# Kernel optimization log

Measured on AMD Instinct MI355X. Metric: run time of the kernel, lower is better.

## Reference

```python
import jax, jax.numpy as jnp
import numpy as np

N, E = 50000, 800000          # nodes, directed edges
F_IN = 80                     # 16 unique sensors * 5 features
H, C = 4, 96                  # num_heads, hidden_dim
D = H * C                     # 384 = concat output dim per GAT layer
NC = 20                       # n_classes = number of components
NEG_SLOPE = 0.2               # PyG GATv2Conv default negative_slope
EPS = 1e-5                    # LayerNorm eps


def layer_norm(x, g, b):
    mu = x.mean(-1, keepdims=True)
    var = x.var(-1, keepdims=True)
    return (x - mu) * jax.lax.rsqrt(var + EPS) * g + b


def gatv2(x, src, dst, Wsrc, Wdst, att, bias):
    # GATv2Conv (concat=True): e_ij = att . leaky_relu(Wsrc x_j + Wdst x_i),
    # alpha = segment-softmax over dst, out_i = sum_j alpha_ij * (Wsrc x_j)
    n = x.shape[0]
    xs = (x @ Wsrc).reshape(n, H, C)
    xd = (x @ Wdst).reshape(n, H, C)
    m = jax.nn.leaky_relu(xs[src] + xd[dst], NEG_SLOPE)      # [E,H,C]
    e = jnp.einsum('ehc,hc->eh', m, att)                     # [E,H]
    emax = jax.ops.segment_max(e, dst, num_segments=n)       # [N,H]
    ex = jnp.exp(e - emax[dst])
    denom = jax.ops.segment_sum(ex, dst, num_segments=n)
    alpha = ex / (denom[dst] + 1e-16)                        # [E,H]
    out = jax.ops.segment_sum(alpha[:, :, None] * xs[src], dst, num_segments=n)
    return out.reshape(n, D) + bias


def setup_inputs():
    key = jax.random.key(0)
    ks = jax.random.split(key, 16)

    def w(k, shape, fan):
        return (jax.random.normal(k, shape, jnp.float32) / np.float32(np.sqrt(fan)))

    inp = {
        'x': jax.random.normal(ks[0], (N, F_IN), jnp.float32),
        'edge_index': jax.random.randint(ks[1], (2, E), 0, N, jnp.int32),
    }
    dims = [F_IN, D, D]
    i = 2
    for l in range(3):
        inp[f'Wsrc{l}'] = w(ks[i], (dims[l], D), dims[l]); i += 1
        inp[f'Wdst{l}'] = w(ks[i], (dims[l], D), dims[l]); i += 1
        inp[f'att{l}'] = w(ks[i], (H, C), C); i += 1
        inp[f'b{l}'] = jnp.zeros((D,), jnp.float32)
        inp[f'g{l}'] = jnp.ones((D,), jnp.float32)
        inp[f'be{l}'] = jnp.zeros((D,), jnp.float32)
    inp['Wc1'] = w(ks[i], (D, C), D); i += 1
    inp['bc1'] = jnp.zeros((C,), jnp.float32)
    inp['gc'] = jnp.ones((C,), jnp.float32)
    inp['bec'] = jnp.zeros((C,), jnp.float32)
    inp['Wc2'] = w(ks[i], (C, NC), C)
    inp['bc2'] = jnp.zeros((NC,), jnp.float32)
    return inp


def reference(x, edge_index,
              Wsrc0, Wdst0, att0, b0, g0, be0,
              Wsrc1, Wdst1, att1, b1, g1, be1,
              Wsrc2, Wdst2, att2, b2, g2, be2,
              Wc1, bc1, gc, bec, Wc2, bc2):
    src, dst = edge_index[0], edge_index[1]
    layers = [(Wsrc0, Wdst0, att0, b0, g0, be0),
              (Wsrc1, Wdst1, att1, b1, g1, be1),
              (Wsrc2, Wdst2, att2, b2, g2, be2)]
    h = x
    for (Ws, Wd, a, b, g, be) in layers:
        h = gatv2(h, src, dst, Ws, Wd, a, b)
        h = jax.nn.elu(layer_norm(h, g, be))   # dropout: identity in eval mode
    h = jax.nn.relu(h @ Wc1 + bc1)
    h = layer_norm(h, gc, bec)
    return h @ Wc2 + bc2
```

## Files before the change

kernel.cpp:

```cpp
#include <hip/hip_runtime.h>
#include <math.h>

#define D 384
#define NCLS 20
#define FIN 80
#define CH 96

typedef unsigned int u32t;
typedef unsigned short u16t;
typedef __attribute__((ext_vector_type(8))) short bf16x8;
typedef __attribute__((ext_vector_type(4))) float f32x4;

__device__ __forceinline__ u16t f2bf(float f) {
    u32t b = __float_as_uint(f);
    u32t r = (b + 0x7FFFu + ((b >> 16) & 1u)) >> 16;
    return (u16t)r;
}
__device__ __forceinline__ float bfl(u32t u) { return __uint_as_float(u << 16); }
__device__ __forceinline__ float bfh(u32t u) { return __uint_as_float(u & 0xFFFF0000u); }

#define GLOAD16(g, l)                                                            \
    __builtin_amdgcn_global_load_lds(                                            \
        (const __attribute__((address_space(1))) void*)(g),                      \
        (__attribute__((address_space(3))) void*)(l), 16, 0, 0)


__global__ void k_zero(int* p, int n) {
    int i = blockIdx.x * blockDim.x + threadIdx.x;
    if (i < n) p[i] = 0;
}

__global__ void k_hist(const int* __restrict__ dst, int* __restrict__ deg, int E) {
    int i = blockIdx.x * blockDim.x + threadIdx.x;
    if (i < E) atomicAdd(&deg[dst[i]], 1);
}

__global__ __launch_bounds__(256) void k_scan1(const int* __restrict__ deg,
                                               int* __restrict__ offs,
                                               int* __restrict__ bsum, int n) {
    __shared__ int sh[256];
    int t = threadIdx.x, i = blockIdx.x * 256 + t;
    int v = (i < n) ? deg[i] : 0;
    sh[t] = v;
    __syncthreads();
    for (int o = 1; o < 256; o <<= 1) {
        int a = (t >= o) ? sh[t - o] : 0;
        __syncthreads();
        sh[t] += a;
        __syncthreads();
    }
    if (i < n) offs[i] = sh[t] - v;
    if (t == 255) bsum[blockIdx.x] = sh[255];
}

__global__ __launch_bounds__(256) void k_scan2(int* __restrict__ bsum, int nb,
                                               int* __restrict__ offs, int n) {
    __shared__ int sh[256];
    int t = threadIdx.x;
    int v = (t < nb) ? bsum[t] : 0;
    sh[t] = v;
    __syncthreads();
    for (int o = 1; o < 256; o <<= 1) {
        int a = (t >= o) ? sh[t - o] : 0;
        __syncthreads();
        sh[t] += a;
        __syncthreads();
    }
    if (t < nb) bsum[t] = sh[t] - v;
    if (t == 255) offs[n] = sh[255];
}

__global__ __launch_bounds__(256) void k_scan3(int* __restrict__ offs,
                                               int* __restrict__ cursor,
                                               const int* __restrict__ bsum, int n) {
    int i = blockIdx.x * 256 + threadIdx.x;
    if (i < n) {
        int o = offs[i] + bsum[blockIdx.x];
        offs[i] = o;
        cursor[i] = o;
    }
}

__global__ void k_scatter(const int* __restrict__ src, const int* __restrict__ dst,
                          int* __restrict__ cursor, int* __restrict__ csr_srcb, int E) {
    int i = blockIdx.x * blockDim.x + threadIdx.x;
    if (i < E) {
        int p = atomicAdd(&cursor[dst[i]], 1);
        csr_srcb[p] = src[i] * 384;
    }
}


__global__ void k_cvt_x(const float* __restrict__ x, u16t* __restrict__ xbf, int N) {
    int i = blockIdx.x * 256 + threadIdx.x;
    if (i >= N * 96) return;
    int r = i / 96, c = i - r * 96;
    float v = (c < FIN) ? x[r * FIN + c] : 0.f;
    xbf[i] = f2bf(v);
}

__global__ void k_cvt_wT(const float* __restrict__ W, u16t* __restrict__ WT,
                         int K, int Kp) {
    int i = blockIdx.x * 256 + threadIdx.x;
    if (i >= D * Kp) return;
    int c = i / Kp, k = i - c * Kp;
    float v = (k < K) ? W[(size_t)k * D + c] : 0.f;
    WT[i] = f2bf(v);
}

__global__ void k_cvt_wc1T(const float* __restrict__ W, u16t* __restrict__ WT) {
    int i = blockIdx.x * 256 + threadIdx.x;
    if (i >= 128 * D) return;
    int c = i / D, k = i - c * D;
    float v = (c < CH) ? W[(size_t)k * CH + c] : 0.f;
    WT[i] = f2bf(v);
}


__global__ __launch_bounds__(256) void k_mm(const u16t* __restrict__ A,
                                            const u16t* __restrict__ BT,
                                            u16t* __restrict__ C, int Kp, int ostride) {
    __shared__ u16t Al[4][128][8];
    __shared__ u16t Bl[4][128][8];
    const int t = threadIdx.x;
    const int wave = t >> 6, lane = t & 63;
    const int wr = wave >> 1, wc = wave & 1;
    const int bm0 = blockIdx.x * 128;
    const int bn0 = blockIdx.y * 128;
    const int col16 = lane & 15, kc = lane >> 4;

    f32x4 acc[4][4] = {};

    const u16t* asrc0 = A + (size_t)(bm0 + lane) * Kp + wave * 8;
    const u16t* asrc1 = A + (size_t)(bm0 + 64 + lane) * Kp + wave * 8;
    const u16t* bsrc0 = BT + (size_t)(bn0 + lane) * Kp + wave * 8;
    const u16t* bsrc1 = BT + (size_t)(bn0 + 64 + lane) * Kp + wave * 8;
    u16t* alds0 = &Al[wave][0][0];
    u16t* alds1 = &Al[wave][64][0];
    u16t* blds0 = &Bl[wave][0][0];
    u16t* blds1 = &Bl[wave][64][0];

    for (int k0 = 0; k0 < Kp; k0 += 32) {
        GLOAD16(asrc0 + k0, alds0);
        GLOAD16(asrc1 + k0, alds1);
        GLOAD16(bsrc0 + k0, blds0);
        GLOAD16(bsrc1 + k0, blds1);
        __syncthreads();

        bf16x8 a[4], b[4];
#pragma unroll
        for (int m = 0; m < 4; m++)
            a[m] = *(const bf16x8*)&Al[kc][wr * 64 + m * 16 + col16][0];
#pragma unroll
        for (int n = 0; n < 4; n++)
            b[n] = *(const bf16x8*)&Bl[kc][wc * 64 + n * 16 + col16][0];
#pragma unroll
        for (int m = 0; m < 4; m++)
#pragma unroll
            for (int n = 0; n < 4; n++)
                acc[m][n] = __builtin_amdgcn_mfma_f32_16x16x32_bf16(
                    a[m], b[n], acc[m][n], 0, 0, 0);
        __syncthreads();
    }

#pragma unroll
    for (int m = 0; m < 4; m++) {
#pragma unroll
        for (int n = 0; n < 4; n++) {
#pragma unroll
            for (int j = 0; j < 4; j++) {
                int row = bm0 + wr * 64 + m * 16 + (lane >> 4) * 4 + j;
                int col = bn0 + wc * 64 + n * 16 + col16;
                C[(size_t)row * ostride + col] = f2bf(acc[m][n][j]);
            }
        }
    }
}


__global__ __launch_bounds__(256) void k_mmh(const u16t* __restrict__ A,
                                             const u16t* __restrict__ BT,
                                             const float* __restrict__ bc1,
                                             float* __restrict__ Yh) {
    __shared__ u16t Al[4][128][8];
    __shared__ u16t Bl[4][128][8];
    const int t = threadIdx.x;
    const int wave = t >> 6, lane = t & 63;
    const int wr = wave >> 1, wc = wave & 1;
    const int bm0 = blockIdx.x * 128;
    const int col16 = lane & 15, kc = lane >> 4;

    f32x4 acc[4][4] = {};

    const u16t* asrc0 = A + (size_t)(bm0 + lane) * D + wave * 8;
    const u16t* asrc1 = A + (size_t)(bm0 + 64 + lane) * D + wave * 8;
    const u16t* bsrc0 = BT + (size_t)lane * D + wave * 8;
    const u16t* bsrc1 = BT + (size_t)(64 + lane) * D + wave * 8;
    u16t* alds0 = &Al[wave][0][0];
    u16t* alds1 = &Al[wave][64][0];
    u16t* blds0 = &Bl[wave][0][0];
    u16t* blds1 = &Bl[wave][64][0];

    for (int k0 = 0; k0 < D; k0 += 32) {
        GLOAD16(asrc0 + k0, alds0);
        GLOAD16(asrc1 + k0, alds1);
        GLOAD16(bsrc0 + k0, blds0);
        GLOAD16(bsrc1 + k0, blds1);
        __syncthreads();

        bf16x8 a[4], b[4];
#pragma unroll
        for (int m = 0; m < 4; m++)
            a[m] = *(const bf16x8*)&Al[kc][wr * 64 + m * 16 + col16][0];
#pragma unroll
        for (int n = 0; n < 4; n++)
            b[n] = *(const bf16x8*)&Bl[kc][wc * 64 + n * 16 + col16][0];
#pragma unroll
        for (int m = 0; m < 4; m++)
#pragma unroll
            for (int n = 0; n < 4; n++)
                acc[m][n] = __builtin_amdgcn_mfma_f32_16x16x32_bf16(
                    a[m], b[n], acc[m][n], 0, 0, 0);
        __syncthreads();
    }

#pragma unroll
    for (int m = 0; m < 4; m++) {
#pragma unroll
        for (int n = 0; n < 4; n++) {
            int col = wc * 64 + n * 16 + col16;
            if (col < CH) {
                float bc = bc1[col];
#pragma unroll
                for (int j = 0; j < 4; j++) {
                    int row = bm0 + wr * 64 + m * 16 + (lane >> 4) * 4 + j;
                    Yh[(size_t)row * CH + col] = fmaxf(acc[m][n][j] + bc, 0.f);
                }
            }
        }
    }
}


__global__ __launch_bounds__(256) void k_gat(const u32t* __restrict__ XSXD,
                                             const float* __restrict__ att,
                                             const float* __restrict__ bias,
                                             const float* __restrict__ gamma,
                                             const float* __restrict__ beta,
                                             const int* __restrict__ offs,
                                             const int* __restrict__ csr_srcb,
                                             u16t* __restrict__ Hout,
                                             int N) {
    int wave = threadIdx.x >> 6;
    int lane = threadIdx.x & 63;
    int node = blockIdx.x * 4 + wave;
    if (node >= N) return;
    int c0 = lane * 6;
    int lo3 = lane * 3;

    const u32t* xdp = XSXD + (size_t)node * 384 + 192 + lo3;
    u32t d0 = xdp[0], d1 = xdp[1], d2 = xdp[2];
    float xd[6] = {bfl(d0), bfh(d0), bfl(d1), bfh(d1), bfl(d2), bfh(d2)};
    float attr[6];
#pragma unroll
    for (int k = 0; k < 6; k++) attr[k] = att[c0 + k];

    float m = -INFINITY, denom = 0.f;
    float acc[6] = {0.f, 0.f, 0.f, 0.f, 0.f, 0.f};
    int e0 = offs[node], e1 = offs[node + 1];

    for (int e = e0; e < e1; e++) {
        const u32t* xsp = XSXD + (u32t)csr_srcb[e] + lo3;
        u32t a0 = xsp[0], a1 = xsp[1], a2 = xsp[2];
        float xs[6] = {bfl(a0), bfh(a0), bfl(a1), bfh(a1), bfl(a2), bfh(a2)};
        float part = 0.f;
#pragma unroll
        for (int k = 0; k < 6; k++) {
            float v = xs[k] + xd[k];
            part = fmaf(fmaxf(v, 0.2f * v), attr[k], part);
        }
#pragma unroll
        for (int o = 1; o < 16; o <<= 1) part += __shfl_xor(part, o, 64);

        if (__builtin_expect(__any(part - m > 8.0f), 0)) {
            float nm = fmaxf(m, part);
            float r = __expf(m - nm);
            float p = __expf(part - nm);
            denom = denom * r + p;
#pragma unroll
            for (int k = 0; k < 6; k++) acc[k] = fmaf(p, xs[k], acc[k] * r);
            m = nm;
        } else {
            float p = __expf(part - m);
            denom += p;
#pragma unroll
            for (int k = 0; k < 6; k++) acc[k] = fmaf(p, xs[k], acc[k]);
        }
    }

    float inv = 1.f / (denom + 1e-16f);
    float v[6];
    float s1 = 0.f;
#pragma unroll
    for (int k = 0; k < 6; k++) { v[k] = acc[k] * inv + bias[c0 + k]; s1 += v[k]; }
#pragma unroll
    for (int o = 1; o < 64; o <<= 1) s1 += __shfl_xor(s1, o, 64);
    float mu = s1 * (1.f / 384.f);
    float s2 = 0.f;
#pragma unroll
    for (int k = 0; k < 6; k++) { float d = v[k] - mu; s2 += d * d; }
#pragma unroll
    for (int o = 1; o < 64; o <<= 1) s2 += __shfl_xor(s2, o, 64);
    float rstd = rsqrtf(s2 * (1.f / 384.f) + 1e-5f);

    float ov[6];
#pragma unroll
    for (int k = 0; k < 6; k++) {
        float y = (v[k] - mu) * rstd * gamma[c0 + k] + beta[c0 + k];
        ov[k] = y > 0.f ? y : expm1f(y);
    }
    u32t w0 = (u32t)f2bf(ov[0]) | ((u32t)f2bf(ov[1]) << 16);
    u32t w1 = (u32t)f2bf(ov[2]) | ((u32t)f2bf(ov[3]) << 16);
    u32t w2 = (u32t)f2bf(ov[4]) | ((u32t)f2bf(ov[5]) << 16);
    u32t* hp = (u32t*)Hout + (size_t)node * 192 + lo3;
    hp[0] = w0; hp[1] = w1; hp[2] = w2;
}


__global__ __launch_bounds__(256) void k_lnout(const float* __restrict__ Yh,
                                               const float* __restrict__ gc,
                                               const float* __restrict__ bec,
                                               const float* __restrict__ Wc2,
                                               const float* __restrict__ bc2,
                                               float* __restrict__ out, int N) {
    __shared__ float w2[CH * NCLS];
    __shared__ float ln[8][CH];
    int t = threadIdx.x;
    int g = t >> 5, tl = t & 31;
    int node = blockIdx.x * 8 + g;

    for (int i = t; i < CH * NCLS; i += 256) w2[i] = Wc2[i];

    if (node < N) {
        const float* yp = Yh + (size_t)node * CH;
        float y0 = yp[tl], y1 = yp[32 + tl], y2 = yp[64 + tl];
        float s = y0 + y1 + y2;
#pragma unroll
        for (int o = 1; o < 32; o <<= 1) s += __shfl_xor(s, o, 32);
        float mu = s * (1.f / CH);
        float d0 = y0 - mu, d1 = y1 - mu, d2 = y2 - mu;
        float q = d0 * d0 + d1 * d1 + d2 * d2;
#pragma unroll
        for (int o = 1; o < 32; o <<= 1) q += __shfl_xor(q, o, 32);
        float rstd = rsqrtf(q * (1.f / CH) + 1e-5f);
        ln[g][tl]      = d0 * rstd * gc[tl]      + bec[tl];
        ln[g][32 + tl] = d1 * rstd * gc[32 + tl] + bec[32 + tl];
        ln[g][64 + tl] = d2 * rstd * gc[64 + tl] + bec[64 + tl];
    }
    __syncthreads();

    if (node < N && tl < NCLS) {
        float o = bc2[tl];
        for (int c = 0; c < CH; c++) o += ln[g][c] * w2[c * NCLS + tl];
        out[(size_t)node * NCLS + tl] = o;
    }
}


extern "C" void kernel_launch(void* const* d_in, const int* in_sizes, int n_in,
                              void* d_out, int out_size, void* d_ws, size_t ws_size,
                              hipStream_t stream) {
    const float* x        = (const float*)d_in[0];
    const int*   eidx     = (const int*)d_in[1];
    const float* Wsrc[3]  = {(const float*)d_in[2],  (const float*)d_in[8],  (const float*)d_in[14]};
    const float* Wdst[3]  = {(const float*)d_in[3],  (const float*)d_in[9],  (const float*)d_in[15]};
    const float* attw[3]  = {(const float*)d_in[4],  (const float*)d_in[10], (const float*)d_in[16]};
    const float* bia[3]   = {(const float*)d_in[5],  (const float*)d_in[11], (const float*)d_in[17]};
    const float* gam[3]   = {(const float*)d_in[6],  (const float*)d_in[12], (const float*)d_in[18]};
    const float* bet[3]   = {(const float*)d_in[7],  (const float*)d_in[13], (const float*)d_in[19]};
    const float* Wc1 = (const float*)d_in[20];
    const float* bc1 = (const float*)d_in[21];
    const float* gc  = (const float*)d_in[22];
    const float* bec = (const float*)d_in[23];
    const float* Wc2 = (const float*)d_in[24];
    const float* bc2 = (const float*)d_in[25];

    const int N = in_sizes[0] / FIN;
    const int E = in_sizes[1] / 2;
    const int Mpad = ((N + 127) / 128) * 128;
    const int* srcp = eidx;
    const int* dstp = eidx + E;

    u16t* xbf  = (u16t*)d_ws;
    u16t* XSXD = xbf + (size_t)Mpad * 96;
    u16t* Hbf  = XSXD + (size_t)Mpad * 768;
    u16t* WT0s = Hbf + (size_t)Mpad * D;
    u16t* WT0d = WT0s + 384 * 96;
    u16t* WT1s = WT0d + 384 * 96;
    u16t* WT1d = WT1s + 384 * 384;
    u16t* WT2s = WT1d + 384 * 384;
    u16t* WT2d = WT2s + 384 * 384;
    u16t* Wc1T = WT2d + 384 * 384;
    float* Yh  = (float*)(Wc1T + 128 * 384);
    int* offs    = (int*)(Yh + (size_t)Mpad * CH);
    int* cursor  = offs + (N + 1);
    int* deg     = cursor + (N + 1);
    int* bsum    = deg + N;
    int* csr_srcb = bsum + 512;

    const int nb = (N + 255) / 256;

    k_zero<<<nb, 256, 0, stream>>>(deg, N);
    k_hist<<<(E + 255) / 256, 256, 0, stream>>>(dstp, deg, E);
    k_scan1<<<nb, 256, 0, stream>>>(deg, offs, bsum, N);
    k_scan2<<<1, 256, 0, stream>>>(bsum, nb, offs, N);
    k_scan3<<<nb, 256, 0, stream>>>(offs, cursor, bsum, N);
    k_scatter<<<(E + 255) / 256, 256, 0, stream>>>(srcp, dstp, cursor, csr_srcb, E);

    k_cvt_x<<<(N * 96 + 255) / 256, 256, 0, stream>>>(x, xbf, N);
    k_cvt_wT<<<(D * 96 + 255) / 256, 256, 0, stream>>>(Wsrc[0], WT0s, FIN, 96);
    k_cvt_wT<<<(D * 96 + 255) / 256, 256, 0, stream>>>(Wdst[0], WT0d, FIN, 96);
    k_cvt_wT<<<(D * D + 255) / 256, 256, 0, stream>>>(Wsrc[1], WT1s, D, D);
    k_cvt_wT<<<(D * D + 255) / 256, 256, 0, stream>>>(Wdst[1], WT1d, D, D);
    k_cvt_wT<<<(D * D + 255) / 256, 256, 0, stream>>>(Wsrc[2], WT2s, D, D);
    k_cvt_wT<<<(D * D + 255) / 256, 256, 0, stream>>>(Wdst[2], WT2d, D, D);
    k_cvt_wc1T<<<(128 * D + 255) / 256, 256, 0, stream>>>(Wc1, Wc1T);

    dim3 gmm(Mpad / 128, 768 / 128);
    int gatGrid = (N + 3) / 4;

    k_mm<<<gmm, 256, 0, stream>>>(xbf, WT0s, XSXD, 96, 768);
    k_gat<<<gatGrid, 256, 0, stream>>>((const u32t*)XSXD, attw[0], bia[0], gam[0], bet[0],
                                       offs, csr_srcb, Hbf, N);
    k_mm<<<gmm, 256, 0, stream>>>(Hbf, WT1s, XSXD, D, 768);
    k_gat<<<gatGrid, 256, 0, stream>>>((const u32t*)XSXD, attw[1], bia[1], gam[1], bet[1],
                                       offs, csr_srcb, Hbf, N);
    k_mm<<<gmm, 256, 0, stream>>>(Hbf, WT2s, XSXD, D, 768);
    k_gat<<<gatGrid, 256, 0, stream>>>((const u32t*)XSXD, attw[2], bia[2], gam[2], bet[2],
                                       offs, csr_srcb, Hbf, N);

    k_mmh<<<Mpad / 128, 256, 0, stream>>>(Hbf, Wc1T, bc1, Yh);
    k_lnout<<<(N + 7) / 8, 256, 0, stream>>>(Yh, gc, bec, Wc2, bc2,
                                             (float*)d_out, N);
}
```

Measured before the change: 865.5 us.

## Prefetch neighbor rows in GAT loop, use exp2 softmax, fuse conversion kernels

The GAT aggregation loop now loads 64 CSR source indices at once, one per lane, and broadcasts them with readlane. The next neighbor's feature row is prefetched while the current one is processed, which hides gather latency and removes the serial index-load dependency. The attention weights are pre-scaled by log2(e) so the softmax can use the hardware exp2, and ELU uses __expf instead of expm1f, trading a little precision near zero. The eight input and weight conversion launches are merged into one kernel to cut launch overhead.

```diff
diff --git a/kernel.cpp b/kernel.cpp
--- a/kernel.cpp
+++ b/kernel.cpp
@@ -91,29 +91,49 @@
 }
 
 
-__global__ void k_cvt_x(const float* __restrict__ x, u16t* __restrict__ xbf, int N) {
+__global__ __launch_bounds__(256) void k_cvt_all(
+    const float* __restrict__ x,
+    const float* __restrict__ Ws0, const float* __restrict__ Wd0,
+    const float* __restrict__ Ws1, const float* __restrict__ Wd1,
+    const float* __restrict__ Ws2, const float* __restrict__ Wd2,
+    const float* __restrict__ Wc1,
+    u16t* __restrict__ xbf,
+    u16t* __restrict__ WT0s, u16t* __restrict__ WT0d,
+    u16t* __restrict__ WT1s, u16t* __restrict__ WT1d,
+    u16t* __restrict__ WT2s, u16t* __restrict__ WT2d,
+    u16t* __restrict__ Wc1T, int N) {
+    const int s96 = 384 * 96, s384 = 384 * 384, sc1 = 128 * 384;
     int i = blockIdx.x * 256 + threadIdx.x;
-    if (i >= N * 96) return;
-    int r = i / 96, c = i - r * 96;
-    float v = (c < FIN) ? x[r * FIN + c] : 0.f;
-    xbf[i] = f2bf(v);
-}
-
-__global__ void k_cvt_wT(const float* __restrict__ W, u16t* __restrict__ WT,
-                         int K, int Kp) {
-    int i = blockIdx.x * 256 + threadIdx.x;
-    if (i >= D * Kp) return;
-    int c = i / Kp, k = i - c * Kp;
-    float v = (k < K) ? W[(size_t)k * D + c] : 0.f;
-    WT[i] = f2bf(v);
-}
-
-__global__ void k_cvt_wc1T(const float* __restrict__ W, u16t* __restrict__ WT) {
-    int i = blockIdx.x * 256 + threadIdx.x;
-    if (i >= 128 * D) return;
-    int c = i / D, k = i - c * D;
-    float v = (c < CH) ? W[(size_t)k * CH + c] : 0.f;
-    WT[i] = f2bf(v);
+
+    int n0 = N * 96;
+    if (i < n0) {
+        int r = i / 96, c = i - r * 96;
+        xbf[i] = f2bf(c < FIN ? x[r * FIN + c] : 0.f);
+        return;
+    }
+    i -= n0;
+    if (i < 2 * s96) {
+        const float* W = (i < s96) ? Ws0 : Wd0;
+        u16t* O = (i < s96) ? WT0s : WT0d;
+        int k2 = (i < s96) ? i : i - s96;
+        int c = k2 / 96, k = k2 - c * 96;
+        O[k2] = f2bf(k < FIN ? W[(size_t)k * D + c] : 0.f);
+        return;
+    }
+    i -= 2 * s96;
+    if (i < 4 * s384) {
+        int w = i / s384, k2 = i - w * s384;
+        const float* W = (w == 0) ? Ws1 : (w == 1) ? Wd1 : (w == 2) ? Ws2 : Wd2;
+        u16t* O = (w == 0) ? WT1s : (w == 1) ? WT1d : (w == 2) ? WT2s : WT2d;
+        int c = k2 / 384, k = k2 - c * 384;
+        O[k2] = f2bf(W[(size_t)k * D + c]);
+        return;
+    }
+    i -= 4 * s384;
+    if (i < sc1) {
+        int c = i / D, k = i - c * D;
+        Wc1T[i] = f2bf(c < CH ? Wc1[(size_t)k * CH + c] : 0.f);
+    }
 }
 
 
@@ -263,38 +283,50 @@
     float xd[6] = {bfl(d0), bfh(d0), bfl(d1), bfh(d1), bfl(d2), bfh(d2)};
     float attr[6];
 #pragma unroll
-    for (int k = 0; k < 6; k++) attr[k] = att[c0 + k];
+    for (int k = 0; k < 6; k++) attr[k] = att[c0 + k] * 1.44269504f;
 
     float m = -INFINITY, denom = 0.f;
     float acc[6] = {0.f, 0.f, 0.f, 0.f, 0.f, 0.f};
     int e0 = offs[node], e1 = offs[node + 1];
 
-    for (int e = e0; e < e1; e++) {
-        const u32t* xsp = XSXD + (u32t)csr_srcb[e] + lo3;
-        u32t a0 = xsp[0], a1 = xsp[1], a2 = xsp[2];
-        float xs[6] = {bfl(a0), bfh(a0), bfl(a1), bfh(a1), bfl(a2), bfh(a2)};
-        float part = 0.f;
-#pragma unroll
-        for (int k = 0; k < 6; k++) {
-            float v = xs[k] + xd[k];
-            part = fmaf(fmaxf(v, 0.2f * v), attr[k], part);
-        }
-#pragma unroll
-        for (int o = 1; o < 16; o <<= 1) part += __shfl_xor(part, o, 64);
-
-        if (__builtin_expect(__any(part - m > 8.0f), 0)) {
-            float nm = fmaxf(m, part);
-            float r = __expf(m - nm);
-            float p = __expf(part - nm);
-            denom = denom * r + p;
-#pragma unroll
-            for (int k = 0; k < 6; k++) acc[k] = fmaf(p, xs[k], acc[k] * r);
-            m = nm;
-        } else {
-            float p = __expf(part - m);
-            denom += p;
-#pragma unroll
-            for (int k = 0; k < 6; k++) acc[k] = fmaf(p, xs[k], acc[k]);
+    for (int base = e0; base < e1; base += 64) {
+        int cnt = min(64, e1 - base);
+        u32t midx = (lane < cnt) ? (u32t)csr_srcb[base + lane] : 0u;
+        u32t off = __builtin_amdgcn_readlane(midx, 0);
+        const u32t* p = XSXD + off + lo3;
+        u32t a0 = p[0], a1 = p[1], a2 = p[2];
+
+        for (int j = 0; j < cnt; j++) {
+            u32t b0 = a0, b1 = a1, b2 = a2;
+            if (j + 1 < cnt) {
+                u32t offn = __builtin_amdgcn_readlane(midx, j + 1);
+                const u32t* pn = XSXD + offn + lo3;
+                a0 = pn[0]; a1 = pn[1]; a2 = pn[2];
+            }
+            float xs[6] = {bfl(b0), bfh(b0), bfl(b1), bfh(b1), bfl(b2), bfh(b2)};
+            float part = 0.f;
+#pragma unroll
+            for (int k = 0; k < 6; k++) {
+                float v = xs[k] + xd[k];
+                part = fmaf(fmaxf(v, 0.2f * v), attr[k], part);
+            }
+#pragma unroll
+            for (int o = 1; o < 16; o <<= 1) part += __shfl_xor(part, o, 64);
+
+            if (__builtin_expect(__any(part - m > 8.0f), 0)) {
+                float nm = fmaxf(m, part);
+                float r = __builtin_amdgcn_exp2f(m - nm);
+                float pp = __builtin_amdgcn_exp2f(part - nm);
+                denom = denom * r + pp;
+#pragma unroll
+                for (int k = 0; k < 6; k++) acc[k] = fmaf(pp, xs[k], acc[k] * r);
+                m = nm;
+            } else {
+                float pp = __builtin_amdgcn_exp2f(part - m);
+                denom += pp;
+#pragma unroll
+                for (int k = 0; k < 6; k++) acc[k] = fmaf(pp, xs[k], acc[k]);
+            }
         }
     }
 
@@ -317,7 +349,7 @@
 #pragma unroll
     for (int k = 0; k < 6; k++) {
         float y = (v[k] - mu) * rstd * gamma[c0 + k] + beta[c0 + k];
-        ov[k] = y > 0.f ? y : expm1f(y);
+        ov[k] = y > 0.f ? y : __expf(y) - 1.f;
     }
     u32t w0 = (u32t)f2bf(ov[0]) | ((u32t)f2bf(ov[1]) << 16);
     u32t w1 = (u32t)f2bf(ov[2]) | ((u32t)f2bf(ov[3]) << 16);
@@ -417,14 +449,13 @@
     k_scan3<<<nb, 256, 0, stream>>>(offs, cursor, bsum, N);
     k_scatter<<<(E + 255) / 256, 256, 0, stream>>>(srcp, dstp, cursor, csr_srcb, E);
 
-    k_cvt_x<<<(N * 96 + 255) / 256, 256, 0, stream>>>(x, xbf, N);
-    k_cvt_wT<<<(D * 96 + 255) / 256, 256, 0, stream>>>(Wsrc[0], WT0s, FIN, 96);
-    k_cvt_wT<<<(D * 96 + 255) / 256, 256, 0, stream>>>(Wdst[0], WT0d, FIN, 96);
-    k_cvt_wT<<<(D * D + 255) / 256, 256, 0, stream>>>(Wsrc[1], WT1s, D, D);
-    k_cvt_wT<<<(D * D + 255) / 256, 256, 0, stream>>>(Wdst[1], WT1d, D, D);
-    k_cvt_wT<<<(D * D + 255) / 256, 256, 0, stream>>>(Wsrc[2], WT2s, D, D);
-    k_cvt_wT<<<(D * D + 255) / 256, 256, 0, stream>>>(Wdst[2], WT2d, D, D);
-    k_cvt_wc1T<<<(128 * D + 255) / 256, 256, 0, stream>>>(Wc1, Wc1T);
+    {
+        long total = (long)N * 96 + 2L * (384 * 96) + 4L * (384 * 384) + 128L * 384;
+        int cblocks = (int)((total + 255) / 256);
+        k_cvt_all<<<cblocks, 256, 0, stream>>>(
+            x, Wsrc[0], Wdst[0], Wsrc[1], Wdst[1], Wsrc[2], Wdst[2], Wc1,
+            xbf, WT0s, WT0d, WT1s, WT1d, WT2s, WT2d, Wc1T, N);
+    }
 
     dim3 gmm(Mpad / 128, 768 / 128);
     int gatGrid = (N + 3) / 4;
```

New measurement: 749.8 us. -13.4%, faster.
